# Performance work log

Hardware: AMD Instinct MI355X
Metric: run time of the kernel (lower is better)

Reference implementation:

```python
import jax, jax.numpy as jnp
import numpy as np

N_NODES = 100000
BN_EPS = 1e-5


def _gcn_layer(x, W, b, row, col, ew):
    # support = x @ W  (dense GEMM), then sparse aggregation: out[r] += w * support[c]
    support = x @ W
    msgs = ew[:, None] * support[col]            # [E, out_dim] gather
    agg = jax.ops.segment_sum(msgs, row, num_segments=N_NODES)
    return agg + b


def _batch_norm(x):
    # fresh BatchNorm1d each call: training-mode batch stats, gamma=1, beta=0
    mean = jnp.mean(x, axis=0, keepdims=True)
    var = jnp.var(x, axis=0, keepdims=True)      # biased variance, as in BN
    return (x - mean) * jax.lax.rsqrt(var + BN_EPS)


def setup_inputs() -> dict:
    key = jax.random.key(0)
    ks = jax.random.split(key, 10)
    nfeat, nhid, nclass = 512, 256, 64
    E = 3200000
    x = jax.random.normal(ks[0], (N_NODES, nfeat), dtype=jnp.float32)
    edge_index = jax.random.randint(ks[1], (2, E), 0, N_NODES, dtype=jnp.int32)
    edge_weight = jax.random.uniform(ks[2], (E,), dtype=jnp.float32)
    def glorot(k, fan_in, fan_out):
        s = 1.0 / np.sqrt(fan_in)
        return jax.random.uniform(k, (fan_in, fan_out), dtype=jnp.float32, minval=-s, maxval=s)
    W1 = glorot(ks[3], nfeat, nhid)
    b1 = jnp.zeros((nhid,), dtype=jnp.float32)
    W2 = glorot(ks[4], nhid, nhid)
    b2 = jnp.zeros((nhid,), dtype=jnp.float32)
    W3 = glorot(ks[5], nhid, nclass)
    b3 = jnp.zeros((nclass,), dtype=jnp.float32)
    return {"x": x, "edge_index": edge_index, "edge_weight": edge_weight,
            "W1": W1, "b1": b1, "W2": W2, "b2": b2, "W3": W3, "b3": b3}


def reference(x, edge_index, edge_weight, W1, b1, W2, b2, W3, b3):
    row, col = edge_index[0], edge_index[1]
    h = _batch_norm(jax.nn.relu(_gcn_layer(x, W1, b1, row, col, edge_weight)))
    h = _batch_norm(jax.nn.relu(_gcn_layer(h, W2, b2, row, col, edge_weight)))
    h = jax.nn.relu(_gcn_layer(h, W3, b3, row, col, edge_weight))
    return h
```

## Files before the change

### kernel.cpp

```cpp
#include <hip/hip_runtime.h>

#define THREADS 256
#define BSH 8
#define EPB 8192

typedef _Float16 f16;
typedef _Float16 f16x8 __attribute__((ext_vector_type(8)));
typedef _Float16 f16x4 __attribute__((ext_vector_type(4)));
typedef float f32x4 __attribute__((ext_vector_type(4)));


__global__ void k_scan1(const int* __restrict__ cnt, int* __restrict__ outp,
                        int* __restrict__ bsum, int n) {
  __shared__ int sh[256];
  int t = threadIdx.x;
  int base = blockIdx.x * 1024 + t * 4;
  int v[4];
#pragma unroll
  for (int j = 0; j < 4; ++j) {
    int idx = base + j;
    v[j] = (idx < n) ? cnt[idx] : 0;
  }
  int tot = v[0] + v[1] + v[2] + v[3];
  sh[t] = tot;
  __syncthreads();
  for (int off = 1; off < 256; off <<= 1) {
    int x = 0;
    if (t >= off) x = sh[t - off];
    __syncthreads();
    sh[t] += x;
    __syncthreads();
  }
  if (t == 255) bsum[blockIdx.x] = sh[255];
  int run = sh[t] - tot;
#pragma unroll
  for (int j = 0; j < 4; ++j) {
    int idx = base + j;
    if (idx < n) outp[idx] = run;
    run += v[j];
  }
}

__global__ void k_scan2(int* __restrict__ bsum, int nb) {
  __shared__ int sh[256];
  int t = threadIdx.x;
  int v = (t < nb) ? bsum[t] : 0;
  sh[t] = v;
  __syncthreads();
  for (int off = 1; off < 256; off <<= 1) {
    int x = 0;
    if (t >= off) x = sh[t - off];
    __syncthreads();
    sh[t] += x;
    __syncthreads();
  }
  if (t < nb) bsum[t] = sh[t] - v;
}

__global__ void k_scan3(int* __restrict__ outp, const int* __restrict__ bsum,
                        int n, int total) {
  int base = blockIdx.x * 1024 + threadIdx.x * 4;
  int add = bsum[blockIdx.x];
#pragma unroll
  for (int j = 0; j < 4; ++j) {
    int idx = base + j;
    if (idx < n) outp[idx] += add;
  }
  if (blockIdx.x == 0 && threadIdx.x == 0) outp[n] = total;
}


__global__ __launch_bounds__(256) void k_hist_convW(
    const int* __restrict__ rows, int* __restrict__ cnt2d, int e, int nblk, int nb,
    const float* __restrict__ W, f16* __restrict__ Wt, int K, int N,
    float* __restrict__ statZero) {
  int t = threadIdx.x;
  if (blockIdx.x < nblk) {
    __shared__ int hist[512];
    int blk = blockIdx.x;
    for (int i = t; i < nb; i += 256) hist[i] = 0;
    __syncthreads();
    int eb = blk * EPB;
#pragma unroll 4
    for (int it = 0; it < 32; ++it) {
      int i = eb + it * 256 + t;
      if (i < e) atomicAdd(&hist[rows[i] >> BSH], 1);
    }
    __syncthreads();
    for (int i = t; i < nb; i += 256) cnt2d[i * nblk + blk] = hist[i];
  } else {
    int cb = blockIdx.x - nblk;
    if (cb == 0) {
#pragma unroll
      for (int j = 0; j < 6; ++j) statZero[j * 256 + t] = 0.f;
    }
    int i = cb * 256 + t;
    if (i < N * K) {
      int n = i / K, k = i - n * K;
      Wt[i] = (f16)W[(size_t)k * N + n];
    }
  }
}

__global__ __launch_bounds__(256) void k_bin(
    const int* __restrict__ rows, const int* __restrict__ cols,
    const float* __restrict__ w, const int* __restrict__ off2d,
    int2* __restrict__ temp, int e, int nblk, int nb) {
  __shared__ int base[512];
  __shared__ int cursor[512];
  int blk = blockIdx.x, t = threadIdx.x;
  for (int i = t; i < nb; i += 256) {
    base[i] = off2d[i * nblk + blk];
    cursor[i] = 0;
  }
  __syncthreads();
  int eb = blk * EPB;
#pragma unroll 4
  for (int it = 0; it < 32; ++it) {
    int i = eb + it * 256 + t;
    if (i < e) {
      int r = rows[i];
      int b = r >> BSH;
      int pos = base[b] + atomicAdd(&cursor[b], 1);
      temp[pos] = make_int2(((r & 255) << 17) | cols[i], __float_as_int(w[i]));
    }
  }
}

__global__ __launch_bounds__(256) void k_scatter(
    const int2* __restrict__ temp, const int* __restrict__ off2d,
    int* __restrict__ rowptr, int2* __restrict__ ed,
    int n, int e, int nblk, int nb) {
  __shared__ int rowCnt[256];
  __shared__ int rowBase[256];
  __shared__ int rowCur[256];
  int b = blockIdx.x, t = threadIdx.x;
  int r0 = b << BSH;
  int nr = min(256, n - r0);
  int start = off2d[b * nblk];
  int end = off2d[(b + 1) * nblk];
  rowCnt[t] = 0;
  __syncthreads();
  for (int p = start + t; p < end; p += 256)
    atomicAdd(&rowCnt[temp[p].x >> 17], 1);
  __syncthreads();
  int v = rowCnt[t];
  rowBase[t] = v;
  __syncthreads();
  for (int off = 1; off < 256; off <<= 1) {
    int x = 0;
    if (t >= off) x = rowBase[t - off];
    __syncthreads();
    rowBase[t] += x;
    __syncthreads();
  }
  int excl = rowBase[t] - v;
  __syncthreads();
  rowBase[t] = excl;
  rowCur[t] = 0;
  if (t < nr) rowptr[r0 + t] = start + excl;
  if (b == nb - 1 && t == 0) rowptr[n] = e;
  __syncthreads();
  for (int p = start + t; p < end; p += 256) {
    int2 ei = temp[p];
    int ro = ei.x >> 17;
    int slot = start + rowBase[ro] + atomicAdd(&rowCur[ro], 1);
    ed[slot] = make_int2(ei.x & 0x1FFFF, ei.y);
  }
}


__global__ __launch_bounds__(256) void k_bnfold(
    const float* __restrict__ W, const float* __restrict__ sums,
    f16* __restrict__ Wt, float* __restrict__ biasRow, int K, int N, int n) {
  __shared__ float sc[256], sf[256];
  int t = threadIdx.x;
  if (t < K) {
    float inv = 1.0f / (float)n;
    float mean = sums[t] * inv;
    float var = sums[256 + t] * inv - mean * mean;
    float rstd = rsqrtf(var + 1e-5f);
    sc[t] = rstd;
    sf[t] = -mean * rstd;
  }
  __syncthreads();
  int i = blockIdx.x * 256 + t;
  if (i < N * K) {
    int nn = i / K, k = i - nn * K;
    Wt[i] = (f16)(sc[k] * W[(size_t)k * N + nn]);
  }
  if (blockIdx.x < (K >> 4) && t < N) {
    int k0 = blockIdx.x * 16;
    float s = 0.f;
#pragma unroll
    for (int j = 0; j < 16; ++j) s += sf[k0 + j] * W[(size_t)(k0 + j) * N + t];
    atomicAdd(&biasRow[t], s);
  }
}


template <int BN, bool AF16>
__global__ __launch_bounds__(256) void k_gemm_mfma(
    const void* __restrict__ Ap, const f16* __restrict__ Wt,
    const float* __restrict__ biasRow, f16* __restrict__ Csup, int M, int K) {
  constexpr int BM = 128;
  constexpr int BK = 32;
  constexpr int LDT = BK + 8;
  __shared__ __align__(16) f16 As[BM][LDT];
  __shared__ __align__(16) f16 Bs[BN][LDT];

  const int tid = threadIdx.x;
  const int wave = tid >> 6;
  const int lane = tid & 63;
  const int m0 = blockIdx.x * BM;
  constexpr int WM = (BN == 256) ? 8 : 2;
  constexpr int WN = 4;
  const int wrow = (BN == 256) ? 0 : wave * 32;
  const int wcol = (BN == 256) ? wave * 64 : 0;
  const int l15 = lane & 15;
  const int lq = lane >> 4;

  const int arow = tid >> 1;
  const int akofs = (tid & 1) * 16;
  const int srow = tid >> 2;
  const int skofs = (tid & 3) * 8;
  constexpr int BROWS = BN / 64;

  f32x4 acc[WM][WN] = {};

  for (int k0 = 0; k0 < K; k0 += BK) {
    f16x8 a16[2];
    int gr = m0 + arow;
    if constexpr (AF16) {
      if (gr < M) {
        const f16* ap = (const f16*)Ap + (size_t)gr * K + k0 + akofs;
        a16[0] = *(const f16x8*)ap;
        a16[1] = *(const f16x8*)(ap + 8);
      } else {
#pragma unroll
        for (int j = 0; j < 8; ++j) { a16[0][j] = (f16)0.f; a16[1][j] = (f16)0.f; }
      }
    } else {
      float va[16];
      if (gr < M) {
        const float* ap = (const float*)Ap + (size_t)gr * K + k0 + akofs;
#pragma unroll
        for (int q = 0; q < 4; ++q) *(float4*)&va[q * 4] = *(const float4*)(ap + q * 4);
      } else {
#pragma unroll
        for (int j = 0; j < 16; ++j) va[j] = 0.f;
      }
#pragma unroll
      for (int j = 0; j < 8; ++j) { a16[0][j] = (f16)va[j]; a16[1][j] = (f16)va[8 + j]; }
    }

    f16x8 vb[BROWS];
#pragma unroll
    for (int j = 0; j < BROWS; ++j)
      vb[j] = *(const f16x8*)(Wt + (size_t)(srow + j * 64) * K + k0 + skofs);

    __syncthreads();
    *(f16x8*)&As[arow][akofs] = a16[0];
    *(f16x8*)&As[arow][akofs + 8] = a16[1];
#pragma unroll
    for (int j = 0; j < BROWS; ++j) *(f16x8*)&Bs[srow + j * 64][skofs] = vb[j];
    __syncthreads();

    f16x8 af[WM], bf[WN];
#pragma unroll
    for (int m = 0; m < WM; ++m)
      af[m] = *(const f16x8*)&As[wrow + m * 16 + l15][lq * 8];
#pragma unroll
    for (int n = 0; n < WN; ++n)
      bf[n] = *(const f16x8*)&Bs[wcol + n * 16 + l15][lq * 8];
#pragma unroll
    for (int m = 0; m < WM; ++m)
#pragma unroll
      for (int n = 0; n < WN; ++n)
        acc[m][n] = __builtin_amdgcn_mfma_f32_16x16x32_f16(af[m], bf[n], acc[m][n], 0, 0, 0);
  }

  float bb[WN];
#pragma unroll
  for (int n = 0; n < WN; ++n)
    bb[n] = biasRow ? biasRow[wcol + n * 16 + l15] : 0.f;

#pragma unroll
  for (int m = 0; m < WM; ++m) {
#pragma unroll
    for (int r = 0; r < 4; ++r) {
      int row = m0 + wrow + m * 16 + lq * 4 + r;
      if (row < M) {
        f16* cp = Csup + (size_t)row * BN + wcol + l15;
#pragma unroll
        for (int n = 0; n < WN; ++n) cp[n * 16] = (f16)(acc[m][n][r] + bb[n]);
      }
    }
  }
}


__global__ __launch_bounds__(256) void k_agg256(
    const f16* __restrict__ sup, const int* __restrict__ rowptr,
    const int2* __restrict__ ed, const float* __restrict__ bias,
    f16* __restrict__ out, int n) {
  int wid = (blockIdx.x * THREADS + threadIdx.x) >> 6;
  int lane = threadIdx.x & 63;
  if (wid >= n) return;
  int p0 = rowptr[wid], p1 = rowptr[wid + 1];

  const f16x4* supv = (const f16x4*)sup;
  float acc[4][4] = {};
  int p = p0;
  for (; p + 16 <= p1; p += 16) {
    int2 e[16];
#pragma unroll
    for (int j = 0; j < 16; ++j) e[j] = ed[p + j];
    f16x4 v[16];
#pragma unroll
    for (int j = 0; j < 16; ++j) v[j] = supv[(size_t)e[j].x * 64 + lane];
#pragma unroll
    for (int j = 0; j < 16; ++j) {
      float wt = __int_as_float(e[j].y);
      acc[j & 3][0] += wt * (float)v[j][0];
      acc[j & 3][1] += wt * (float)v[j][1];
      acc[j & 3][2] += wt * (float)v[j][2];
      acc[j & 3][3] += wt * (float)v[j][3];
    }
  }
  for (; p + 4 <= p1; p += 4) {
    int2 e[4];
#pragma unroll
    for (int j = 0; j < 4; ++j) e[j] = ed[p + j];
    f16x4 v[4];
#pragma unroll
    for (int j = 0; j < 4; ++j) v[j] = supv[(size_t)e[j].x * 64 + lane];
#pragma unroll
    for (int j = 0; j < 4; ++j) {
      float wt = __int_as_float(e[j].y);
      acc[j][0] += wt * (float)v[j][0];
      acc[j][1] += wt * (float)v[j][1];
      acc[j][2] += wt * (float)v[j][2];
      acc[j][3] += wt * (float)v[j][3];
    }
  }
  for (; p < p1; ++p) {
    int2 e0 = ed[p];
    float wt = __int_as_float(e0.y);
    f16x4 v = supv[(size_t)e0.x * 64 + lane];
    acc[0][0] += wt * (float)v[0];
    acc[0][1] += wt * (float)v[1];
    acc[0][2] += wt * (float)v[2];
    acc[0][3] += wt * (float)v[3];
  }
  float4 b = *(const float4*)(bias + lane * 4);
  f16x4 r;
  r[0] = (f16)fmaxf(acc[0][0] + acc[1][0] + acc[2][0] + acc[3][0] + b.x, 0.f);
  r[1] = (f16)fmaxf(acc[0][1] + acc[1][1] + acc[2][1] + acc[3][1] + b.y, 0.f);
  r[2] = (f16)fmaxf(acc[0][2] + acc[1][2] + acc[2][2] + acc[3][2] + b.z, 0.f);
  r[3] = (f16)fmaxf(acc[0][3] + acc[1][3] + acc[2][3] + acc[3][3] + b.w, 0.f);
  *(f16x4*)(out + (size_t)wid * 256 + lane * 4) = r;
}


__global__ __launch_bounds__(256) void k_agg64(
    const f16* __restrict__ sup, const int* __restrict__ rowptr,
    const int2* __restrict__ ed, const float* __restrict__ bias,
    float* __restrict__ out, int n) {
  int wid = (blockIdx.x * THREADS + threadIdx.x) >> 6;
  int lane = threadIdx.x & 63;
  if (wid >= n) return;
  int p0 = rowptr[wid], p1 = rowptr[wid + 1];
  int q = lane >> 4;
  int hl = lane & 15;

  const f16x4* supv = (const f16x4*)sup;
  float acc[2][4] = {};
  int p = p0;
  for (; p + 32 <= p1; p += 32) {
    int2 e[8];
#pragma unroll
    for (int j = 0; j < 8; ++j) e[j] = ed[p + 4 * j + q];
    f16x4 v[8];
#pragma unroll
    for (int j = 0; j < 8; ++j) v[j] = supv[(size_t)e[j].x * 16 + hl];
#pragma unroll
    for (int j = 0; j < 8; ++j) {
      float wt = __int_as_float(e[j].y);
      acc[j & 1][0] += wt * (float)v[j][0];
      acc[j & 1][1] += wt * (float)v[j][1];
      acc[j & 1][2] += wt * (float)v[j][2];
      acc[j & 1][3] += wt * (float)v[j][3];
    }
  }
  for (; p + 4 <= p1; p += 4) {
    int2 e0 = ed[p + q];
    float wt = __int_as_float(e0.y);
    f16x4 v = supv[(size_t)e0.x * 16 + hl];
    acc[0][0] += wt * (float)v[0];
    acc[0][1] += wt * (float)v[1];
    acc[0][2] += wt * (float)v[2];
    acc[0][3] += wt * (float)v[3];
  }
  if (p < p1) {
    int idx = p + q;
    int c = 0;
    float wt = 0.f;
    if (idx < p1) {
      int2 e0 = ed[idx];
      c = e0.x;
      wt = __int_as_float(e0.y);
    }
    f16x4 v = supv[(size_t)c * 16 + hl];
    acc[0][0] += wt * (float)v[0];
    acc[0][1] += wt * (float)v[1];
    acc[0][2] += wt * (float)v[2];
    acc[0][3] += wt * (float)v[3];
  }
  float t0 = acc[0][0] + acc[1][0];
  float t1 = acc[0][1] + acc[1][1];
  float t2 = acc[0][2] + acc[1][2];
  float t3 = acc[0][3] + acc[1][3];
  t0 += __shfl_xor(t0, 16); t0 += __shfl_xor(t0, 32);
  t1 += __shfl_xor(t1, 16); t1 += __shfl_xor(t1, 32);
  t2 += __shfl_xor(t2, 16); t2 += __shfl_xor(t2, 32);
  t3 += __shfl_xor(t3, 16); t3 += __shfl_xor(t3, 32);
  if (q == 0) {
    float4 b = *(const float4*)(bias + hl * 4);
    float4 res;
    res.x = fmaxf(t0 + b.x, 0.f);
    res.y = fmaxf(t1 + b.y, 0.f);
    res.z = fmaxf(t2 + b.z, 0.f);
    res.w = fmaxf(t3 + b.w, 0.f);
    *(float4*)(out + (size_t)wid * 64 + hl * 4) = res;
  }
}


__global__ __launch_bounds__(256) void k_colstats(const f16* __restrict__ y,
                                                  float* __restrict__ sums, int n) {
  __shared__ float sh[8][256];
  int t = threadIdx.x;
  int cg = (t & 31) * 8;
  int rs = t >> 5;
  float s[8] = {}, s2[8] = {};
  for (int r = blockIdx.x * 8 + rs; r < n; r += gridDim.x * 8) {
    f16x8 v = *(const f16x8*)(y + (size_t)r * 256 + cg);
#pragma unroll
    for (int j = 0; j < 8; ++j) {
      float f = (float)v[j];
      s[j] += f;
      s2[j] += f * f;
    }
  }
#pragma unroll
  for (int j = 0; j < 8; ++j) sh[rs][cg + j] = s[j];
  __syncthreads();
  float tot = 0.f;
#pragma unroll
  for (int k = 0; k < 8; ++k) tot += sh[k][t];
  atomicAdd(&sums[t], tot);
  __syncthreads();
#pragma unroll
  for (int j = 0; j < 8; ++j) sh[rs][cg + j] = s2[j];
  __syncthreads();
  tot = 0.f;
#pragma unroll
  for (int k = 0; k < 8; ++k) tot += sh[k][t];
  atomicAdd(&sums[256 + t], tot);
}


extern "C" void kernel_launch(void* const* d_in, const int* in_sizes, int n_in,
                              void* d_out, int out_size, void* d_ws, size_t ws_size,
                              hipStream_t stream) {
  const float* x = (const float*)d_in[0];
  const int* ei = (const int*)d_in[1];
  const float* ew = (const float*)d_in[2];
  const float* W1 = (const float*)d_in[3];
  const float* b1 = (const float*)d_in[4];
  const float* W2 = (const float*)d_in[5];
  const float* b2 = (const float*)d_in[6];
  const float* W3 = (const float*)d_in[7];
  const float* b3 = (const float*)d_in[8];
  float* out = (float*)d_out;

  const int N = in_sizes[0] / 512;
  const int E = in_sizes[2];

  const int NB = (N + 255) >> BSH;
  const int NBLK = (E + EPB - 1) / EPB;
  const int scanN = NB * NBLK;

  char* p = (char*)d_ws;
  auto alloc = [&](size_t bytes) {
    void* r = (void*)p;
    p += (bytes + 255) & ~(size_t)255;
    return r;
  };
  int* rowptr = (int*)alloc((size_t)(N + 1) * 4);
  int* cnt2d = (int*)alloc((size_t)scanN * 4);
  int* off2d = (int*)alloc((size_t)(scanN + 1) * 4);
  int* bsum = (int*)alloc(4096);
  float* statZ = (float*)alloc(1536 * 4);
  float* sumsA = statZ;
  float* sumsB = statZ + 512;
  float* biasRowA = statZ + 1024;
  float* biasRowB = statZ + 1280;
  f16* Wt1 = (f16*)alloc((size_t)512 * 256 * 2);
  f16* Wt2 = (f16*)alloc((size_t)256 * 256 * 2);
  f16* Wt3 = (f16*)alloc((size_t)256 * 64 * 2);
  int2* temp = (int2*)alloc((size_t)E * 8);
  int2* ed = (int2*)alloc((size_t)E * 8);
  f16* sup = (f16*)alloc((size_t)N * 256 * 2);
  f16* act = (f16*)alloc((size_t)N * 256 * 2);

  const int* rows = ei;
  const int* colsIn = ei + E;

  const int convBlocks = (512 * 256 + 255) / 256;
  k_hist_convW<<<NBLK + convBlocks, 256, 0, stream>>>(
      rows, cnt2d, E, NBLK, NB, W1, Wt1, 512, 256, statZ);
  int nbs = (scanN + 1023) / 1024;
  k_scan1<<<nbs, 256, 0, stream>>>(cnt2d, off2d, bsum, scanN);
  k_scan2<<<1, 256, 0, stream>>>(bsum, nbs);
  k_scan3<<<nbs, 256, 0, stream>>>(off2d, bsum, scanN, E);
  k_bin<<<NBLK, 256, 0, stream>>>(rows, colsIn, ew, off2d, temp, E, NBLK, NB);
  k_scatter<<<NB, 256, 0, stream>>>(temp, off2d, rowptr, ed, N, E, NBLK, NB);

  const int gemmBlocks = (N + 127) / 128;
  const int aggBlocks = (N * 64 + THREADS - 1) / THREADS;

  k_gemm_mfma<256, false><<<gemmBlocks, 256, 0, stream>>>(x, Wt1, nullptr, sup, N, 512);
  k_agg256<<<aggBlocks, 256, 0, stream>>>(sup, rowptr, ed, b1, act, N);

  k_colstats<<<240, 256, 0, stream>>>(act, sumsA, N);
  k_bnfold<<<(256 * 256 + 255) / 256, 256, 0, stream>>>(W2, sumsA, Wt2, biasRowA, 256, 256, N);

  k_gemm_mfma<256, true><<<gemmBlocks, 256, 0, stream>>>(act, Wt2, biasRowA, sup, N, 256);
  k_agg256<<<aggBlocks, 256, 0, stream>>>(sup, rowptr, ed, b2, act, N);

  k_colstats<<<240, 256, 0, stream>>>(act, sumsB, N);
  k_bnfold<<<(256 * 64 + 255) / 256, 256, 0, stream>>>(W3, sumsB, Wt3, biasRowB, 256, 64, N);

  k_gemm_mfma<64, true><<<gemmBlocks, 256, 0, stream>>>(act, Wt3, biasRowB, sup, N, 256);
  k_agg64<<<aggBlocks, 256, 0, stream>>>(sup, rowptr, ed, b3, out, N);
}
```

Baseline: 884.6 us.

## Fuse edge binning with first GEMM and use decoupled-lookback scan

Replaces the three-kernel scan with a single decoupled-lookback scan that uses per-tile status words, zeroed in the histogram kernel. Edge binning and the first layer's x@W1 GEMM now run in one launch, with blocks split by index, so the two independent jobs can overlap. Bucket size drops from 256 to 128 rows, which doubles the number of buckets and shrinks per-block scatter work. The lookback relies on earlier tiles being scheduled first and spins on global atomics, and the merged kernel carries the larger GEMM shared-memory footprint into the binning blocks.

```diff
diff --git a/kernel.cpp b/kernel.cpp
--- a/kernel.cpp
+++ b/kernel.cpp
@@ -1,7 +1,7 @@
 #include <hip/hip_runtime.h>
 
 #define THREADS 256
-#define BSH 8
+#define BSH 7
 #define EPB 8192
 
 typedef _Float16 f16;
@@ -10,73 +10,13 @@
 typedef float f32x4 __attribute__((ext_vector_type(4)));
 
 
-__global__ void k_scan1(const int* __restrict__ cnt, int* __restrict__ outp,
-                        int* __restrict__ bsum, int n) {
-  __shared__ int sh[256];
-  int t = threadIdx.x;
-  int base = blockIdx.x * 1024 + t * 4;
-  int v[4];
-#pragma unroll
-  for (int j = 0; j < 4; ++j) {
-    int idx = base + j;
-    v[j] = (idx < n) ? cnt[idx] : 0;
-  }
-  int tot = v[0] + v[1] + v[2] + v[3];
-  sh[t] = tot;
-  __syncthreads();
-  for (int off = 1; off < 256; off <<= 1) {
-    int x = 0;
-    if (t >= off) x = sh[t - off];
-    __syncthreads();
-    sh[t] += x;
-    __syncthreads();
-  }
-  if (t == 255) bsum[blockIdx.x] = sh[255];
-  int run = sh[t] - tot;
-#pragma unroll
-  for (int j = 0; j < 4; ++j) {
-    int idx = base + j;
-    if (idx < n) outp[idx] = run;
-    run += v[j];
-  }
-}
-
-__global__ void k_scan2(int* __restrict__ bsum, int nb) {
-  __shared__ int sh[256];
-  int t = threadIdx.x;
-  int v = (t < nb) ? bsum[t] : 0;
-  sh[t] = v;
-  __syncthreads();
-  for (int off = 1; off < 256; off <<= 1) {
-    int x = 0;
-    if (t >= off) x = sh[t - off];
-    __syncthreads();
-    sh[t] += x;
-    __syncthreads();
-  }
-  if (t < nb) bsum[t] = sh[t] - v;
-}
-
-__global__ void k_scan3(int* __restrict__ outp, const int* __restrict__ bsum,
-                        int n, int total) {
-  int base = blockIdx.x * 1024 + threadIdx.x * 4;
-  int add = bsum[blockIdx.x];
-#pragma unroll
-  for (int j = 0; j < 4; ++j) {
-    int idx = base + j;
-    if (idx < n) outp[idx] += add;
-  }
-  if (blockIdx.x == 0 && threadIdx.x == 0) outp[n] = total;
-}
-
-
 __global__ __launch_bounds__(256) void k_hist_convW(
     const int* __restrict__ rows, int* __restrict__ cnt2d, int e, int nblk, int nb,
     const float* __restrict__ W, f16* __restrict__ Wt, int K, int N,
-    float* __restrict__ statZero) {
+    float* __restrict__ statZero, unsigned long long* __restrict__ tpub, int ntiles) {
   int t = threadIdx.x;
   if (blockIdx.x < nblk) {
-    __shared__ int hist[512];
+    __shared__ int hist[1024];
     int blk = blockIdx.x;
     for (int i = t; i < nb; i += 256) hist[i] = 0;
     __syncthreads();
@@ -93,6 +33,7 @@
     if (cb == 0) {
 #pragma unroll
       for (int j = 0; j < 6; ++j) statZero[j * 256 + t] = 0.f;
+      for (int i = t; i < ntiles; i += 256) tpub[i] = 0ULL;
     }
     int i = cb * 256 + t;
     if (i < N * K) {
@@ -102,63 +43,244 @@
   }
 }
 
-__global__ __launch_bounds__(256) void k_bin(
+
+__global__ __launch_bounds__(256) void k_scanDL(
+    const int* __restrict__ cnt, int* __restrict__ outp,
+    unsigned long long* __restrict__ tpub, int n) {
+  __shared__ int sh[256];
+  __shared__ int sPrefix;
+  int tile = blockIdx.x, t = threadIdx.x;
+  int base = tile * 1024 + t * 4;
+  int v[4];
+#pragma unroll
+  for (int j = 0; j < 4; ++j) {
+    int idx = base + j;
+    v[j] = (idx < n) ? cnt[idx] : 0;
+  }
+  int tot = v[0] + v[1] + v[2] + v[3];
+  sh[t] = tot;
+  __syncthreads();
+  for (int off = 1; off < 256; off <<= 1) {
+    int x = 0;
+    if (t >= off) x = sh[t - off];
+    __syncthreads();
+    sh[t] += x;
+    __syncthreads();
+  }
+  int blockTot = sh[255];
+  int run = sh[t] - tot;
+
+  if (t == 0) {
+    if (tile == 0) {
+      sPrefix = 0;
+      atomicExch(&tpub[0], ((unsigned long long)(unsigned)blockTot << 2) | 2ULL);
+    } else {
+      atomicExch(&tpub[tile], ((unsigned long long)(unsigned)blockTot << 2) | 1ULL);
+      long long sum = 0;
+      int pred = tile - 1;
+      while (true) {
+        unsigned long long s = atomicAdd(&tpub[pred], 0ULL);
+        unsigned st = (unsigned)(s & 3ULL);
+        if (st == 2) { sum += (long long)(s >> 2); break; }
+        if (st == 1) { sum += (long long)(s >> 2); --pred; }
+      }
+      sPrefix = (int)sum;
+      atomicExch(&tpub[tile],
+                 ((unsigned long long)(unsigned)(sum + blockTot) << 2) | 2ULL);
+    }
+  }
+  __syncthreads();
+  int pfx = sPrefix;
+#pragma unroll
+  for (int j = 0; j < 4; ++j) {
+    int idx = base + j;
+    if (idx < n) outp[idx] = run + pfx;
+    run += v[j];
+  }
+  if (tile == gridDim.x - 1 && t == 0) outp[n] = pfx + blockTot;
+}
+
+
+template <int BN, bool AF16>
+__device__ __forceinline__ void gemm_dev(
+    int mblk, const void* __restrict__ Ap, const f16* __restrict__ Wt,
+    const float* __restrict__ biasRow, f16* __restrict__ Csup, int M, int K,
+    char* smem) {
+  constexpr int BM = 128;
+  constexpr int BK = 32;
+  constexpr int LDT = BK + 8;
+  f16 (*As)[LDT] = (f16(*)[LDT])smem;
+  f16 (*Bs)[LDT] = (f16(*)[LDT])(smem + BM * LDT * 2);
+
+  const int tid = threadIdx.x;
+  const int wave = tid >> 6;
+  const int lane = tid & 63;
+  const int m0 = mblk * BM;
+  constexpr int WM = (BN == 256) ? 8 : 2;
+  constexpr int WN = 4;
+  const int wrow = (BN == 256) ? 0 : wave * 32;
+  const int wcol = (BN == 256) ? wave * 64 : 0;
+  const int l15 = lane & 15;
+  const int lq = lane >> 4;
+
+  const int arow = tid >> 1;
+  const int akofs = (tid & 1) * 16;
+  const int srow = tid >> 2;
+  const int skofs = (tid & 3) * 8;
+  constexpr int BROWS = BN / 64;
+
+  f32x4 acc[WM][WN] = {};
+
+  for (int k0 = 0; k0 < K; k0 += BK) {
+    f16x8 a16[2];
+    int gr = m0 + arow;
+    if constexpr (AF16) {
+      if (gr < M) {
+        const f16* ap = (const f16*)Ap + (size_t)gr * K + k0 + akofs;
+        a16[0] = *(const f16x8*)ap;
+        a16[1] = *(const f16x8*)(ap + 8);
+      } else {
+#pragma unroll
+        for (int j = 0; j < 8; ++j) { a16[0][j] = (f16)0.f; a16[1][j] = (f16)0.f; }
+      }
+    } else {
+      float va[16];
+      if (gr < M) {
+        const float* ap = (const float*)Ap + (size_t)gr * K + k0 + akofs;
+#pragma unroll
+        for (int q = 0; q < 4; ++q) *(float4*)&va[q * 4] = *(const float4*)(ap + q * 4);
+      } else {
+#pragma unroll
+        for (int j = 0; j < 16; ++j) va[j] = 0.f;
+      }
+#pragma unroll
+      for (int j = 0; j < 8; ++j) { a16[0][j] = (f16)va[j]; a16[1][j] = (f16)va[8 + j]; }
+    }
+
+    f16x8 vb[BROWS];
+#pragma unroll
+    for (int j = 0; j < BROWS; ++j)
+      vb[j] = *(const f16x8*)(Wt + (size_t)(srow + j * 64) * K + k0 + skofs);
+
+    __syncthreads();
+    *(f16x8*)&As[arow][akofs] = a16[0];
+    *(f16x8*)&As[arow][akofs + 8] = a16[1];
+#pragma unroll
+    for (int j = 0; j < BROWS; ++j) *(f16x8*)&Bs[srow + j * 64][skofs] = vb[j];
+    __syncthreads();
+
+    f16x8 af[WM], bf[WN];
+#pragma unroll
+    for (int m = 0; m < WM; ++m)
+      af[m] = *(const f16x8*)&As[wrow + m * 16 + l15][lq * 8];
+#pragma unroll
+    for (int n = 0; n < WN; ++n)
+      bf[n] = *(const f16x8*)&Bs[wcol + n * 16 + l15][lq * 8];
+#pragma unroll
+    for (int m = 0; m < WM; ++m)
+#pragma unroll
+      for (int n = 0; n < WN; ++n)
+        acc[m][n] = __builtin_amdgcn_mfma_f32_16x16x32_f16(af[m], bf[n], acc[m][n], 0, 0, 0);
+  }
+
+  float bb[WN];
+#pragma unroll
+  for (int n = 0; n < WN; ++n)
+    bb[n] = biasRow ? biasRow[wcol + n * 16 + l15] : 0.f;
+
+#pragma unroll
+  for (int m = 0; m < WM; ++m) {
+#pragma unroll
+    for (int r = 0; r < 4; ++r) {
+      int row = m0 + wrow + m * 16 + lq * 4 + r;
+      if (row < M) {
+        f16* cp = Csup + (size_t)row * BN + wcol + l15;
+#pragma unroll
+        for (int n = 0; n < WN; ++n) cp[n * 16] = (f16)(acc[m][n][r] + bb[n]);
+      }
+    }
+  }
+}
+
+template <int BN, bool AF16>
+__global__ __launch_bounds__(256) void k_gemm_mfma(
+    const void* __restrict__ Ap, const f16* __restrict__ Wt,
+    const float* __restrict__ biasRow, f16* __restrict__ Csup, int M, int K) {
+  __shared__ __align__(16) char smem[(128 + BN) * 40 * 2];
+  gemm_dev<BN, AF16>(blockIdx.x, Ap, Wt, biasRow, Csup, M, K, smem);
+}
+
+
+__global__ __launch_bounds__(256) void k_bin_gemm(
     const int* __restrict__ rows, const int* __restrict__ cols,
     const float* __restrict__ w, const int* __restrict__ off2d,
-    int2* __restrict__ temp, int e, int nblk, int nb) {
-  __shared__ int base[512];
-  __shared__ int cursor[512];
-  int blk = blockIdx.x, t = threadIdx.x;
-  for (int i = t; i < nb; i += 256) {
-    base[i] = off2d[i * nblk + blk];
-    cursor[i] = 0;
-  }
-  __syncthreads();
-  int eb = blk * EPB;
+    int2* __restrict__ temp, int e, int nblk, int nb,
+    const float* __restrict__ x, const f16* __restrict__ Wt1,
+    f16* __restrict__ sup, int M) {
+  __shared__ __align__(16) char smem[(128 + 256) * 40 * 2];
+  int t = threadIdx.x;
+  if (blockIdx.x < nblk) {
+    int* base = (int*)smem;
+    int* cursor = (int*)smem + 1024;
+    int blk = blockIdx.x;
+    for (int i = t; i < nb; i += 256) {
+      base[i] = off2d[i * nblk + blk];
+      cursor[i] = 0;
+    }
+    __syncthreads();
+    int eb = blk * EPB;
 #pragma unroll 4
-  for (int it = 0; it < 32; ++it) {
-    int i = eb + it * 256 + t;
-    if (i < e) {
-      int r = rows[i];
-      int b = r >> BSH;
-      int pos = base[b] + atomicAdd(&cursor[b], 1);
-      temp[pos] = make_int2(((r & 255) << 17) | cols[i], __float_as_int(w[i]));
-    }
-  }
-}
+    for (int it = 0; it < 32; ++it) {
+      int i = eb + it * 256 + t;
+      if (i < e) {
+        int r = rows[i];
+        int b = r >> BSH;
+        int pos = base[b] + atomicAdd(&cursor[b], 1);
+        temp[pos] = make_int2(((r & 127) << 17) | cols[i], __float_as_int(w[i]));
+      }
+    }
+  } else {
+    gemm_dev<256, false>(blockIdx.x - nblk, x, Wt1, nullptr, sup, M, 512, smem);
+  }
+}
+
 
 __global__ __launch_bounds__(256) void k_scatter(
     const int2* __restrict__ temp, const int* __restrict__ off2d,
     int* __restrict__ rowptr, int2* __restrict__ ed,
     int n, int e, int nblk, int nb) {
-  __shared__ int rowCnt[256];
-  __shared__ int rowBase[256];
-  __shared__ int rowCur[256];
+  __shared__ int rowCnt[128];
+  __shared__ int rowBase[128];
+  __shared__ int rowCur[128];
   int b = blockIdx.x, t = threadIdx.x;
   int r0 = b << BSH;
-  int nr = min(256, n - r0);
+  int nr = min(128, n - r0);
   int start = off2d[b * nblk];
   int end = off2d[(b + 1) * nblk];
-  rowCnt[t] = 0;
+  if (t < 128) rowCnt[t] = 0;
   __syncthreads();
   for (int p = start + t; p < end; p += 256)
     atomicAdd(&rowCnt[temp[p].x >> 17], 1);
   __syncthreads();
-  int v = rowCnt[t];
-  rowBase[t] = v;
-  __syncthreads();
-  for (int off = 1; off < 256; off <<= 1) {
+  int v = 0;
+  if (t < 128) {
+    v = rowCnt[t];
+    rowBase[t] = v;
+  }
+  __syncthreads();
+  for (int off = 1; off < 128; off <<= 1) {
     int x = 0;
-    if (t >= off) x = rowBase[t - off];
-    __syncthreads();
-    rowBase[t] += x;
-    __syncthreads();
-  }
-  int excl = rowBase[t] - v;
-  __syncthreads();
-  rowBase[t] = excl;
-  rowCur[t] = 0;
-  if (t < nr) rowptr[r0 + t] = start + excl;
+    if (t < 128 && t >= off) x = rowBase[t - off];
+    __syncthreads();
+    if (t < 128) rowBase[t] += x;
+    __syncthreads();
+  }
+  if (t < 128) {
+    int excl = rowBase[t] - v;
+    rowBase[t] = excl;
+    rowCur[t] = 0;
+    if (t < nr) rowptr[r0 + t] = start + excl;
+  }
   if (b == nb - 1 && t == 0) rowptr[n] = e;
   __syncthreads();
   for (int p = start + t; p < end; p += 256) {
@@ -195,107 +317,6 @@
 #pragma unroll
     for (int j = 0; j < 16; ++j) s += sf[k0 + j] * W[(size_t)(k0 + j) * N + t];
     atomicAdd(&biasRow[t], s);
-  }
-}
-
-
-template <int BN, bool AF16>
-__global__ __launch_bounds__(256) void k_gemm_mfma(
-    const void* __restrict__ Ap, const f16* __restrict__ Wt,
-    const float* __restrict__ biasRow, f16* __restrict__ Csup, int M, int K) {
-  constexpr int BM = 128;
-  constexpr int BK = 32;
-  constexpr int LDT = BK + 8;
-  __shared__ __align__(16) f16 As[BM][LDT];
-  __shared__ __align__(16) f16 Bs[BN][LDT];
-
-  const int tid = threadIdx.x;
-  const int wave = tid >> 6;
-  const int lane = tid & 63;
-  const int m0 = blockIdx.x * BM;
-  constexpr int WM = (BN == 256) ? 8 : 2;
-  constexpr int WN = 4;
-  const int wrow = (BN == 256) ? 0 : wave * 32;
-  const int wcol = (BN == 256) ? wave * 64 : 0;
-  const int l15 = lane & 15;
-  const int lq = lane >> 4;
-
-  const int arow = tid >> 1;
-  const int akofs = (tid & 1) * 16;
-  const int srow = tid >> 2;
-  const int skofs = (tid & 3) * 8;
-  constexpr int BROWS = BN / 64;
-
-  f32x4 acc[WM][WN] = {};
-
-  for (int k0 = 0; k0 < K; k0 += BK) {
-    f16x8 a16[2];
-    int gr = m0 + arow;
-    if constexpr (AF16) {
-      if (gr < M) {
-        const f16* ap = (const f16*)Ap + (size_t)gr * K + k0 + akofs;
-        a16[0] = *(const f16x8*)ap;
-        a16[1] = *(const f16x8*)(ap + 8);
-      } else {
-#pragma unroll
-        for (int j = 0; j < 8; ++j) { a16[0][j] = (f16)0.f; a16[1][j] = (f16)0.f; }
-      }
-    } else {
-      float va[16];
-      if (gr < M) {
-        const float* ap = (const float*)Ap + (size_t)gr * K + k0 + akofs;
-#pragma unroll
-        for (int q = 0; q < 4; ++q) *(float4*)&va[q * 4] = *(const float4*)(ap + q * 4);
-      } else {
-#pragma unroll
-        for (int j = 0; j < 16; ++j) va[j] = 0.f;
-      }
-#pragma unroll
-      for (int j = 0; j < 8; ++j) { a16[0][j] = (f16)va[j]; a16[1][j] = (f16)va[8 + j]; }
-    }
-
-    f16x8 vb[BROWS];
-#pragma unroll
-    for (int j = 0; j < BROWS; ++j)
-      vb[j] = *(const f16x8*)(Wt + (size_t)(srow + j * 64) * K + k0 + skofs);
-
-    __syncthreads();
-    *(f16x8*)&As[arow][akofs] = a16[0];
-    *(f16x8*)&As[arow][akofs + 8] = a16[1];
-#pragma unroll
-    for (int j = 0; j < BROWS; ++j) *(f16x8*)&Bs[srow + j * 64][skofs] = vb[j];
-    __syncthreads();
-
-    f16x8 af[WM], bf[WN];
-#pragma unroll
-    for (int m = 0; m < WM; ++m)
-      af[m] = *(const f16x8*)&As[wrow + m * 16 + l15][lq * 8];
-#pragma unroll
-    for (int n = 0; n < WN; ++n)
-      bf[n] = *(const f16x8*)&Bs[wcol + n * 16 + l15][lq * 8];
-#pragma unroll
-    for (int m = 0; m < WM; ++m)
-#pragma unroll
-      for (int n = 0; n < WN; ++n)
-        acc[m][n] = __builtin_amdgcn_mfma_f32_16x16x32_f16(af[m], bf[n], acc[m][n], 0, 0, 0);
-  }
-
-  float bb[WN];
-#pragma unroll
-  for (int n = 0; n < WN; ++n)
-    bb[n] = biasRow ? biasRow[wcol + n * 16 + l15] : 0.f;
-
-#pragma unroll
-  for (int m = 0; m < WM; ++m) {
-#pragma unroll
-    for (int r = 0; r < 4; ++r) {
-      int row = m0 + wrow + m * 16 + lq * 4 + r;
-      if (row < M) {
-        f16* cp = Csup + (size_t)row * BN + wcol + l15;
-#pragma unroll
-        for (int n = 0; n < WN; ++n) cp[n * 16] = (f16)(acc[m][n][r] + bb[n]);
-      }
-    }
   }
 }
 
@@ -488,9 +509,10 @@
   const int N = in_sizes[0] / 512;
   const int E = in_sizes[2];
 
-  const int NB = (N + 255) >> BSH;
+  const int NB = (N + 127) >> BSH;
   const int NBLK = (E + EPB - 1) / EPB;
   const int scanN = NB * NBLK;
+  const int ntiles = (scanN + 1023) / 1024;
 
   char* p = (char*)d_ws;
   auto alloc = [&](size_t bytes) {
@@ -501,7 +523,7 @@
   int* rowptr = (int*)alloc((size_t)(N + 1) * 4);
   int* cnt2d = (int*)alloc((size_t)scanN * 4);
   int* off2d = (int*)alloc((size_t)(scanN + 1) * 4);
-  int* bsum = (int*)alloc(4096);
+  unsigned long long* tpub = (unsigned long long*)alloc((size_t)ntiles * 8);
   float* statZ = (float*)alloc(1536 * 4);
   float* sumsA = statZ;
   float* sumsB = statZ + 512;
@@ -518,20 +540,20 @@
   const int* rows = ei;
   const int* colsIn = ei + E;
 
-  const int convBlocks = (512 * 256 + 255) / 256;
-  k_hist_convW<<<NBLK + convBlocks, 256, 0, stream>>>(
-      rows, cnt2d, E, NBLK, NB, W1, Wt1, 512, 256, statZ);
-  int nbs = (scanN + 1023) / 1024;
-  k_scan1<<<nbs, 256, 0, stream>>>(cnt2d, off2d, bsum, scanN);
-  k_scan2<<<1, 256, 0, stream>>>(bsum, nbs);
-  k_scan3<<<nbs, 256, 0, stream>>>(off2d, bsum, scanN, E);
-  k_bin<<<NBLK, 256, 0, stream>>>(rows, colsIn, ew, off2d, temp, E, NBLK, NB);
-  k_scatter<<<NB, 256, 0, stream>>>(temp, off2d, rowptr, ed, N, E, NBLK, NB);
-
   const int gemmBlocks = (N + 127) / 128;
   const int aggBlocks = (N * 64 + THREADS - 1) / THREADS;
-
-  k_gemm_mfma<256, false><<<gemmBlocks, 256, 0, stream>>>(x, Wt1, nullptr, sup, N, 512);
+  const int convBlocks = (512 * 256 + 255) / 256;
+
+  k_hist_convW<<<NBLK + convBlocks, 256, 0, stream>>>(
+      rows, cnt2d, E, NBLK, NB, W1, Wt1, 512, 256, statZ, tpub, ntiles);
+
+  k_scanDL<<<ntiles, 256, 0, stream>>>(cnt2d, off2d, tpub, scanN);
+
+  k_bin_gemm<<<NBLK + gemmBlocks, 256, 0, stream>>>(
+      rows, colsIn, ew, off2d, temp, E, NBLK, NB, x, Wt1, sup, N);
+
+  k_scatter<<<NB, 256, 0, stream>>>(temp, off2d, rowptr, ed, N, E, NBLK, NB);
+
   k_agg256<<<aggBlocks, 256, 0, stream>>>(sup, rowptr, ed, b1, act, N);
 
   k_colstats<<<240, 256, 0, stream>>>(act, sumsA, N);
```

Result: no change. 873.4 us (median of 2 runs) (-1.3%).
